# Performance work log

Measured on AMD Instinct MI355X. Metric: run time of the kernel, lower is better.

Reference implementation:

```python
import jax, jax.numpy as jnp
import numpy as np

NEG = -10000.0
EPS = 1e-5

B, N, H, DEPTH = 4096, 64, 128, 3
H2 = H // 2


def setup_inputs() -> dict:
    key = jax.random.key(0)
    k1, k2, k3 = jax.random.split(key, 3)
    hidden_states = jax.random.normal(k1, (B, N, H), dtype=jnp.float32)
    li_vector_num = jax.random.randint(k2, (B,), 0, N + 1, dtype=jnp.int32)
    Ws = jax.random.normal(k3, (DEPTH, H, H2), dtype=jnp.float32) * (1.0 / np.sqrt(H))
    bs = jnp.zeros((DEPTH, H2), dtype=jnp.float32)
    ln_w = jnp.ones((DEPTH, H2), dtype=jnp.float32)
    ln_b = jnp.zeros((DEPTH, H2), dtype=jnp.float32)
    return {"hidden_states": hidden_states, "li_vector_num": li_vector_num,
            "Ws": Ws, "bs": bs, "ln_w": ln_w, "ln_b": ln_b}


def _subgraph(hidden_states, Ws, bs, ln_w, ln_b, li_vector_num):
    b, n, h = hidden_states.shape
    # padding mask: -10000 for invalid vectors (i >= li_vector_num), per polyline
    pad = jnp.where(jnp.arange(n)[None, :] >= li_vector_num[:, None], NEG, 0.0)
    pad = pad.astype(hidden_states.dtype)[:, :, None]  # [B,N,1]
    hs = hidden_states
    for l in range(Ws.shape[0]):
        # MLP: linear -> layernorm -> relu
        x = jnp.einsum('bnh,hk->bnk', hs, Ws[l]) + bs[l]
        mu = jnp.mean(x, axis=-1, keepdims=True)
        var = jnp.mean((x - mu) ** 2, axis=-1, keepdims=True)
        x = ln_w[l] * (x - mu) * jax.lax.rsqrt(var + EPS) + ln_b[l]
        enc = jax.nn.relu(x)  # [B,N,H2]
        m = enc + pad  # masked encoded states
        # leave-one-out max over vector dim via top-2 trick (replaces O(N^2) loop)
        top2 = jax.lax.top_k(jnp.swapaxes(m, 1, 2), 2)[0]  # [B,H2,2]
        top1b = top2[..., 0][:, None, :]  # [B,1,H2]
        top2b = top2[..., 1][:, None, :]  # [B,1,H2]
        loo = jnp.where(m == top1b, top2b, top1b)  # max over i != j
        loo = jnp.maximum(loo, m + NEG)            # faithful: j itself at -10000
        loo = jnp.maximum(loo, 0.0)                # torch.max(max_hidden, zeros)
        hs = jnp.concatenate([enc, loo], axis=-1)  # [B,N,H]
    return jnp.max(hs, axis=1)  # [B,H]


def reference(hidden_states, li_vector_num, Ws, bs, ln_w, ln_b):
    return _subgraph(hidden_states, Ws, bs, ln_w, ln_b, li_vector_num)
```

## Files before the change

kernel.cpp:

```cpp
#include <hip/hip_runtime.h>
#include <hip/hip_bf16.h>

#define NEGV (-10000.0f)
#define EPSV (1e-5f)
#define NINF (-3.4e38f)

typedef __attribute__((ext_vector_type(8))) short short8;
typedef __attribute__((ext_vector_type(4))) float floatx4;

constexpr int Bsz = 4096, Nv = 64, Hd = 128, DEPTH = 3, H2 = 64;
constexpr int ESTR = 72;

struct alignas(8) BH4 { __hip_bfloat162 a, b; };

__device__ __forceinline__ unsigned short f2b(float f) {
    unsigned int u = __builtin_bit_cast(unsigned int, f);
    u += 0x7fffu + ((u >> 16) & 1u);
    return (unsigned short)(u >> 16);
}
__device__ __forceinline__ float b2f(short s) {
    unsigned int u = ((unsigned int)(unsigned short)s) << 16;
    return __builtin_bit_cast(float, u);
}

template <int CTRL>
__device__ __forceinline__ float dpp_add(float v) {
    int y = __builtin_amdgcn_update_dpp(0, __builtin_bit_cast(int, v), CTRL, 0xf, 0xf, true);
    return v + __builtin_bit_cast(float, y);
}
__device__ __forceinline__ float sum16(float v) {
    v = dpp_add<0xB1>(v);
    v = dpp_add<0x4E>(v);
    v = dpp_add<0x124>(v);
    v = dpp_add<0x128>(v);
    return v;
}

__device__ __forceinline__ void t2ins(float& t1, float& t2, float v) {
    float lo = fminf(t1, v); t1 = fmaxf(t1, v); t2 = fmaxf(t2, lo);
}
__device__ __forceinline__ void t2merge(float& t1, float& t2, float o1, float o2) {
    float lo = fminf(t1, o1); t1 = fmaxf(t1, o1); t2 = fmaxf(fmaxf(t2, o2), lo);
}

__global__ void prep_w(const float* __restrict__ Ws, unsigned short* __restrict__ wt) {
    int idx = blockIdx.x * 256 + threadIdx.x;
    if (idx < DEPTH * 8192) {
        int l = idx >> 13, o = idx & 8191;
        int j = o & 7, q = (o >> 3) & 63, hi = (o >> 9) & 3, kt = o >> 11;
        int k = kt * 32 + hi * 8 + j;
        int srccol = (q & 15) * 4 + (q >> 4);
        wt[idx] = f2b(Ws[l * 8192 + k * 64 + srccol]);
    }
}

__global__ __launch_bounds__(256, 3)
void subgraph_kernel(const float* __restrict__ hidden, const int* __restrict__ lvn,
                     const unsigned short* __restrict__ wt,
                     const float* __restrict__ bsv, const float* __restrict__ lnw,
                     const float* __restrict__ lnb, float* __restrict__ out)
{
    __shared__ __hip_bfloat16 encs[2][4][16][ESTR];
    __shared__ float fbuf3[4][4][2][2][64];
    __shared__ float2 mbuf[2][64];
    __shared__ float obuf[2][4][128];

    const int t = threadIdx.x;
    const int lane = t & 63, wid = t >> 6;
    const int b0 = blockIdx.x * 2;
    const int lr = lane & 15, hi = lane >> 4;
    const int L0 = lvn[b0], L1 = lvn[b0 + 1];
    const int arow = wid * 16 + lr;
    const float mA[2] = {(arow >= L0) ? NEGV : 0.0f, (arow >= L1) ? NEGV : 0.0f};

    const float4* ab0 = (const float4*)(hidden + (size_t)b0 * Nv * Hd);
    const float4* ab1 = ab0 + (Nv * Hd) / 4;

    float em[2][4], lm[2][4];

#pragma unroll
    for (int l = 0; l < DEPTH; ++l) {
        const short8* wfrag = (const short8*)(wt + l * 8192);

        short8 af[2][4];
        if (l == 0) {
#pragma unroll
            for (int p = 0; p < 2; ++p) {
                const float4* ab = p ? ab1 : ab0;
#pragma unroll
                for (int kt = 0; kt < 4; ++kt) {
                    int fi = arow * 32 + kt * 8 + hi * 2;
                    float4 f0 = ab[fi], f1 = ab[fi + 1];
                    union { short8 s; __hip_bfloat162 h[4]; } u;
                    u.h[0] = __float22bfloat162_rn(make_float2(f0.x, f0.y));
                    u.h[1] = __float22bfloat162_rn(make_float2(f0.z, f0.w));
                    u.h[2] = __float22bfloat162_rn(make_float2(f1.x, f1.y));
                    u.h[3] = __float22bfloat162_rn(make_float2(f1.z, f1.w));
                    af[p][kt] = u.s;
                }
            }
        } else {
#pragma unroll
            for (int p = 0; p < 2; ++p) {
                af[p][0] = *(const short8*)&encs[p][wid][lr][hi * 8];
                af[p][1] = *(const short8*)&encs[p][wid][lr][32 + hi * 8];
            }
#pragma unroll
            for (int kt = 2; kt < 4; ++kt) {
                int base = (kt - 2) * 16 + hi * 4;
#pragma unroll
                for (int p = 0; p < 2; ++p) {
                    const float4* mq = (const float4*)mbuf[p];
                    float4 q0 = mq[base + 0], q1 = mq[base + 1];
                    float4 q2 = mq[base + 2], q3 = mq[base + 3];
                    float f1s[8] = {q0.x, q0.z, q1.x, q1.z, q2.x, q2.z, q3.x, q3.z};
                    float f2s[8] = {q0.y, q0.w, q1.y, q1.w, q2.y, q2.w, q3.y, q3.w};
                    short8 e = *(const short8*)&encs[p][wid][lr][(kt - 2) * 32 + hi * 8];
                    float lo[8];
#pragma unroll
                    for (int j = 0; j < 8; ++j) {
                        float m = b2f(e[j]) + mA[p];
                        float sel = (m == f1s[j]) ? f2s[j] : f1s[j];
                        lo[j] = fmaxf(sel, 0.0f);
                    }
                    union { short8 s; __hip_bfloat162 h[4]; } u;
                    u.h[0] = __float22bfloat162_rn(make_float2(lo[0], lo[1]));
                    u.h[1] = __float22bfloat162_rn(make_float2(lo[2], lo[3]));
                    u.h[2] = __float22bfloat162_rn(make_float2(lo[4], lo[5]));
                    u.h[3] = __float22bfloat162_rn(make_float2(lo[6], lo[7]));
                    af[p][kt] = u.s;
                }
            }
        }

        floatx4 acc[2][4];
#pragma unroll
        for (int p = 0; p < 2; ++p)
#pragma unroll
            for (int ct = 0; ct < 4; ++ct) { floatx4 z = {0.f, 0.f, 0.f, 0.f}; acc[p][ct] = z; }
#pragma unroll
        for (int kt = 0; kt < 4; ++kt)
#pragma unroll
            for (int ct = 0; ct < 4; ++ct) {
                short8 bf = wfrag[(kt * 4 + hi) * 64 + ct * 16 + lr];
                acc[0][ct] = __builtin_amdgcn_mfma_f32_16x16x32_bf16(af[0][kt], bf, acc[0][ct], 0, 0, 0);
                acc[1][ct] = __builtin_amdgcn_mfma_f32_16x16x32_bf16(af[1][kt], bf, acc[1][ct], 0, 0, 0);
            }

        float4 bias = *(const float4*)(bsv + l * H2 + 4 * lr);
        float4 gwv  = *(const float4*)(lnw + l * H2 + 4 * lr);
        float4 gbv  = *(const float4*)(lnb + l * H2 + 4 * lr);
#pragma unroll
        for (int p = 0; p < 2; ++p)
#pragma unroll
            for (int reg = 0; reg < 4; ++reg) {
                float x0 = acc[p][0][reg] + bias.x;
                float x1 = acc[p][1][reg] + bias.y;
                float x2 = acc[p][2][reg] + bias.z;
                float x3 = acc[p][3][reg] + bias.w;
                float s = sum16((x0 + x1) + (x2 + x3));
                float q = sum16((x0 * x0 + x1 * x1) + (x2 * x2 + x3 * x3));
                float mu  = s * (1.0f / 64.0f);
                float var = fmaxf(q * (1.0f / 64.0f) - mu * mu, 0.0f);
                float rstd = rsqrtf(var + EPSV);
                acc[p][0][reg] = fmaxf(gwv.x * (x0 - mu) * rstd + gbv.x, 0.0f);
                acc[p][1][reg] = fmaxf(gwv.y * (x1 - mu) * rstd + gbv.y, 0.0f);
                acc[p][2][reg] = fmaxf(gwv.z * (x2 - mu) * rstd + gbv.z, 0.0f);
                acc[p][3][reg] = fmaxf(gwv.w * (x3 - mu) * rstd + gbv.w, 0.0f);
            }

        if (l < DEPTH - 1) {
#pragma unroll
            for (int p = 0; p < 2; ++p) {
                const int Lp = p ? L1 : L0;
                float t1v[4] = {NINF, NINF, NINF, NINF}, t2v[4] = {NINF, NINF, NINF, NINF};
#pragma unroll
                for (int reg = 0; reg < 4; ++reg) {
                    float mk = ((wid * 16 + hi * 4 + reg) >= Lp) ? NEGV : 0.0f;
                    BH4 we;
                    we.a = __float22bfloat162_rn(make_float2(acc[p][0][reg], acc[p][1][reg]));
                    we.b = __float22bfloat162_rn(make_float2(acc[p][2][reg], acc[p][3][reg]));
                    *(BH4*)&encs[p][wid][hi * 4 + reg][4 * lr] = we;
                    t2ins(t1v[0], t2v[0], __bfloat162float(we.a.x) + mk);
                    t2ins(t1v[1], t2v[1], __bfloat162float(we.a.y) + mk);
                    t2ins(t1v[2], t2v[2], __bfloat162float(we.b.x) + mk);
                    t2ins(t1v[3], t2v[3], __bfloat162float(we.b.y) + mk);
                }
                *(float4*)&fbuf3[wid][hi][p][0][4 * lr] = make_float4(t1v[0], t1v[1], t1v[2], t1v[3]);
                *(float4*)&fbuf3[wid][hi][p][1][4 * lr] = make_float4(t2v[0], t2v[1], t2v[2], t2v[3]);
            }
        } else {
#pragma unroll
            for (int p = 0; p < 2; ++p) {
                const int Lp = p ? L1 : L0;
                float t1v[4], t2v[4];
#pragma unroll
                for (int ct = 0; ct < 4; ++ct) {
                    float a1 = NINF, a2 = NINF;
#pragma unroll
                    for (int reg = 0; reg < 4; ++reg) {
                        float mk = ((wid * 16 + hi * 4 + reg) >= Lp) ? NEGV : 0.0f;
                        t2ins(a1, a2, acc[p][ct][reg] + mk);
                    }
                    t1v[ct] = a1; t2v[ct] = a2;
                }
                *(float4*)&fbuf3[wid][hi][p][0][4 * lr] = make_float4(t1v[0], t1v[1], t1v[2], t1v[3]);
                *(float4*)&fbuf3[wid][hi][p][1][4 * lr] = make_float4(t2v[0], t2v[1], t2v[2], t2v[3]);
            }
        }
        __syncthreads();

        if (t < 128) {
            int p = t >> 6, c = t & 63;
            float m1 = NINF, m2 = NINF;
#pragma unroll
            for (int w = 0; w < 4; ++w)
#pragma unroll
                for (int h = 0; h < 4; ++h)
                    t2merge(m1, m2, fbuf3[w][h][p][0][c], fbuf3[w][h][p][1][c]);
            mbuf[p][c] = make_float2(m1, m2);
        }
        __syncthreads();

        if (l == DEPTH - 1) {
#pragma unroll
            for (int p = 0; p < 2; ++p) {
                const int Lp = p ? L1 : L0;
                const float4* mq = (const float4*)mbuf[p];
                float4 h0 = mq[2 * lr], h1 = mq[2 * lr + 1];
                float f1v[4] = {h0.x, h0.z, h1.x, h1.z};
                float f2v[4] = {h0.y, h0.w, h1.y, h1.w};
#pragma unroll
                for (int ct = 0; ct < 4; ++ct) {
                    float e0 = NINF, l0 = NINF;
#pragma unroll
                    for (int reg = 0; reg < 4; ++reg) {
                        float e = acc[p][ct][reg];
                        e0 = fmaxf(e0, e);
                        float mk = ((wid * 16 + hi * 4 + reg) >= Lp) ? NEGV : 0.0f;
                        float mv = e + mk;
                        float v = (mv == f1v[ct]) ? f2v[ct] : f1v[ct];
                        l0 = fmaxf(l0, fmaxf(v, 0.0f));
                    }
                    e0 = fmaxf(e0, __shfl_xor(e0, 16, 64));
                    e0 = fmaxf(e0, __shfl_xor(e0, 32, 64));
                    l0 = fmaxf(l0, __shfl_xor(l0, 16, 64));
                    l0 = fmaxf(l0, __shfl_xor(l0, 32, 64));
                    em[p][ct] = e0; lm[p][ct] = l0;
                }
            }
        }
    }

    if (hi == 0) {
#pragma unroll
        for (int p = 0; p < 2; ++p) {
            *(float4*)&obuf[p][wid][4 * lr]      = make_float4(em[p][0], em[p][1], em[p][2], em[p][3]);
            *(float4*)&obuf[p][wid][64 + 4 * lr] = make_float4(lm[p][0], lm[p][1], lm[p][2], lm[p][3]);
        }
    }
    __syncthreads();
    {
        int p = t >> 7, h = t & 127;
        float v = fmaxf(fmaxf(obuf[p][0][h], obuf[p][1][h]), fmaxf(obuf[p][2][h], obuf[p][3][h]));
        out[(size_t)(b0 + p) * Hd + h] = v;
    }
}

extern "C" void kernel_launch(void* const* d_in, const int* in_sizes, int n_in,
                              void* d_out, int out_size, void* d_ws, size_t ws_size,
                              hipStream_t stream) {
    const float* hidden = (const float*)d_in[0];
    const int*   lvn    = (const int*)d_in[1];
    const float* Ws     = (const float*)d_in[2];
    const float* bs     = (const float*)d_in[3];
    const float* lnwp   = (const float*)d_in[4];
    const float* lnbp   = (const float*)d_in[5];
    unsigned short* wt  = (unsigned short*)d_ws;
    float* outp = (float*)d_out;

    prep_w<<<(DEPTH * 8192 + 255) / 256, 256, 0, stream>>>(Ws, wt);
    subgraph_kernel<<<Bsz / 2, 256, 0, stream>>>(hidden, lvn, wt, bs, lnwp, lnbp, outp);
}
```

Measured before the change: 63.73 us.

## Track argmax row for leave-one-out max and simplify final-layer reduction

The top-2 reduction now also records the row index holding the maximum, and the merged per-column maxima are stored pre-rounded to bf16 with the ReLU already applied. Building the leave-one-out operand then only needs an index compare and a byte permute, replacing per-element bf16 decode, mask add, float compare and re-rounding. In the last layer the leave-one-out max collapses to a plain masked max, because the max over rows of the leave-one-out values is just the overall top-1 (or 0 after the ReLU). That removes the second top-2 pass, the shuffles and the extra output staging buffer and barrier. Tie handling shifts from value equality to index identity, and the top-2 is now taken on fp32 values rather than bf16-rounded ones, which can change results slightly.

```diff
diff --git a/kernel.cpp b/kernel.cpp
--- a/kernel.cpp
+++ b/kernel.cpp
@@ -17,10 +17,6 @@
     unsigned int u = __builtin_bit_cast(unsigned int, f);
     u += 0x7fffu + ((u >> 16) & 1u);
     return (unsigned short)(u >> 16);
-}
-__device__ __forceinline__ float b2f(short s) {
-    unsigned int u = ((unsigned int)(unsigned short)s) << 16;
-    return __builtin_bit_cast(float, u);
 }
 
 template <int CTRL>
@@ -36,11 +32,13 @@
     return v;
 }
 
-__device__ __forceinline__ void t2ins(float& t1, float& t2, float v) {
-    float lo = fminf(t1, v); t1 = fmaxf(t1, v); t2 = fmaxf(t2, lo);
-}
-__device__ __forceinline__ void t2merge(float& t1, float& t2, float o1, float o2) {
-    float lo = fminf(t1, o1); t1 = fmaxf(t1, o1); t2 = fmaxf(fmaxf(t2, o2), lo);
+__device__ __forceinline__ void t2insIdx(float& t1, float& t2, unsigned& i1,
+                                         float v, unsigned iv) {
+    bool c = v > t1;
+    float lo = fminf(t1, v);
+    t1 = fmaxf(t1, v);
+    i1 = c ? iv : i1;
+    t2 = fmaxf(t2, lo);
 }
 
 __global__ void prep_w(const float* __restrict__ Ws, unsigned short* __restrict__ wt) {
@@ -61,23 +59,27 @@
                      const float* __restrict__ lnb, float* __restrict__ out)
 {
     __shared__ __hip_bfloat16 encs[2][4][16][ESTR];
-    __shared__ float fbuf3[4][4][2][2][64];
-    __shared__ float2 mbuf[2][64];
-    __shared__ float obuf[2][4][128];
+    __shared__ float fbuf3[4][4][2][3][64];
+    __shared__ float apk[2][64][2];
+    __shared__ unsigned short aidx[2][64];
 
     const int t = threadIdx.x;
     const int lane = t & 63, wid = t >> 6;
     const int b0 = blockIdx.x * 2;
     const int lr = lane & 15, hi = lane >> 4;
     const int L0 = lvn[b0], L1 = lvn[b0 + 1];
-    const int arow = wid * 16 + lr;
-    const float mA[2] = {(arow >= L0) ? NEGV : 0.0f, (arow >= L1) ? NEGV : 0.0f};
+    const unsigned myrow = wid * 16 + lr;
+
+    float madd[2][4];
+#pragma unroll
+    for (int p = 0; p < 2; ++p)
+#pragma unroll
+        for (int reg = 0; reg < 4; ++reg)
+            madd[p][reg] = ((int)(wid * 16 + hi * 4 + reg) >= (p ? L1 : L0)) ? NEGV : 0.0f;
 
     const float4* ab0 = (const float4*)(hidden + (size_t)b0 * Nv * Hd);
     const float4* ab1 = ab0 + (Nv * Hd) / 4;
 
-    float em[2][4], lm[2][4];
-
 #pragma unroll
     for (int l = 0; l < DEPTH; ++l) {
         const short8* wfrag = (const short8*)(wt + l * 8192);
@@ -89,7 +91,7 @@
                 const float4* ab = p ? ab1 : ab0;
 #pragma unroll
                 for (int kt = 0; kt < 4; ++kt) {
-                    int fi = arow * 32 + kt * 8 + hi * 2;
+                    int fi = (int)myrow * 32 + kt * 8 + hi * 2;
                     float4 f0 = ab[fi], f1 = ab[fi + 1];
                     union { short8 s; __hip_bfloat162 h[4]; } u;
                     u.h[0] = __float22bfloat162_rn(make_float2(f0.x, f0.y));
@@ -107,28 +109,33 @@
             }
 #pragma unroll
             for (int kt = 2; kt < 4; ++kt) {
-                int base = (kt - 2) * 16 + hi * 4;
+                int cbase = (kt - 2) * 32 + hi * 8;
 #pragma unroll
                 for (int p = 0; p < 2; ++p) {
-                    const float4* mq = (const float4*)mbuf[p];
-                    float4 q0 = mq[base + 0], q1 = mq[base + 1];
-                    float4 q2 = mq[base + 2], q3 = mq[base + 3];
-                    float f1s[8] = {q0.x, q0.z, q1.x, q1.z, q2.x, q2.z, q3.x, q3.z};
-                    float f2s[8] = {q0.y, q0.w, q1.y, q1.w, q2.y, q2.w, q3.y, q3.w};
-                    short8 e = *(const short8*)&encs[p][wid][lr][(kt - 2) * 32 + hi * 8];
-                    float lo[8];
-#pragma unroll
-                    for (int j = 0; j < 8; ++j) {
-                        float m = b2f(e[j]) + mA[p];
-                        float sel = (m == f1s[j]) ? f2s[j] : f1s[j];
-                        lo[j] = fmaxf(sel, 0.0f);
+                    short8 ar = *(const short8*)&aidx[p][cbase];
+                    const float4* ap = (const float4*)&apk[p][0][0];
+                    int fb = cbase >> 1;
+                    float4 q0 = ap[fb], q1 = ap[fb + 1], q2 = ap[fb + 2], q3 = ap[fb + 3];
+                    unsigned pk1s[8] = {
+                        __builtin_bit_cast(unsigned, q0.x), __builtin_bit_cast(unsigned, q0.z),
+                        __builtin_bit_cast(unsigned, q1.x), __builtin_bit_cast(unsigned, q1.z),
+                        __builtin_bit_cast(unsigned, q2.x), __builtin_bit_cast(unsigned, q2.z),
+                        __builtin_bit_cast(unsigned, q3.x), __builtin_bit_cast(unsigned, q3.z)};
+                    unsigned pk2s[8] = {
+                        __builtin_bit_cast(unsigned, q0.y), __builtin_bit_cast(unsigned, q0.w),
+                        __builtin_bit_cast(unsigned, q1.y), __builtin_bit_cast(unsigned, q1.w),
+                        __builtin_bit_cast(unsigned, q2.y), __builtin_bit_cast(unsigned, q2.w),
+                        __builtin_bit_cast(unsigned, q3.y), __builtin_bit_cast(unsigned, q3.w)};
+                    union { short8 s; unsigned u[4]; } uu;
+#pragma unroll
+                    for (int j2 = 0; j2 < 4; ++j2) {
+                        unsigned s0 = ((unsigned)(unsigned short)ar[2 * j2]     == myrow)
+                                      ? pk2s[2 * j2]     : pk1s[2 * j2];
+                        unsigned s1 = ((unsigned)(unsigned short)ar[2 * j2 + 1] == myrow)
+                                      ? pk2s[2 * j2 + 1] : pk1s[2 * j2 + 1];
+                        uu.u[j2] = __builtin_amdgcn_perm(s1, s0, 0x05040100u);
                     }
-                    union { short8 s; __hip_bfloat162 h[4]; } u;
-                    u.h[0] = __float22bfloat162_rn(make_float2(lo[0], lo[1]));
-                    u.h[1] = __float22bfloat162_rn(make_float2(lo[2], lo[3]));
-                    u.h[2] = __float22bfloat162_rn(make_float2(lo[4], lo[5]));
-                    u.h[3] = __float22bfloat162_rn(make_float2(lo[6], lo[7]));
-                    af[p][kt] = u.s;
+                    af[p][kt] = uu.s;
                 }
             }
         }
@@ -172,98 +179,81 @@
         if (l < DEPTH - 1) {
 #pragma unroll
             for (int p = 0; p < 2; ++p) {
-                const int Lp = p ? L1 : L0;
                 float t1v[4] = {NINF, NINF, NINF, NINF}, t2v[4] = {NINF, NINF, NINF, NINF};
+                unsigned i1v[4] = {0, 0, 0, 0};
 #pragma unroll
                 for (int reg = 0; reg < 4; ++reg) {
-                    float mk = ((wid * 16 + hi * 4 + reg) >= Lp) ? NEGV : 0.0f;
                     BH4 we;
                     we.a = __float22bfloat162_rn(make_float2(acc[p][0][reg], acc[p][1][reg]));
                     we.b = __float22bfloat162_rn(make_float2(acc[p][2][reg], acc[p][3][reg]));
                     *(BH4*)&encs[p][wid][hi * 4 + reg][4 * lr] = we;
-                    t2ins(t1v[0], t2v[0], __bfloat162float(we.a.x) + mk);
-                    t2ins(t1v[1], t2v[1], __bfloat162float(we.a.y) + mk);
-                    t2ins(t1v[2], t2v[2], __bfloat162float(we.b.x) + mk);
-                    t2ins(t1v[3], t2v[3], __bfloat162float(we.b.y) + mk);
+                    float mk = madd[p][reg];
+                    unsigned rowi = wid * 16 + hi * 4 + reg;
+                    t2insIdx(t1v[0], t2v[0], i1v[0], acc[p][0][reg] + mk, rowi);
+                    t2insIdx(t1v[1], t2v[1], i1v[1], acc[p][1][reg] + mk, rowi);
+                    t2insIdx(t1v[2], t2v[2], i1v[2], acc[p][2][reg] + mk, rowi);
+                    t2insIdx(t1v[3], t2v[3], i1v[3], acc[p][3][reg] + mk, rowi);
                 }
                 *(float4*)&fbuf3[wid][hi][p][0][4 * lr] = make_float4(t1v[0], t1v[1], t1v[2], t1v[3]);
                 *(float4*)&fbuf3[wid][hi][p][1][4 * lr] = make_float4(t2v[0], t2v[1], t2v[2], t2v[3]);
-            }
+                *(float4*)&fbuf3[wid][hi][p][2][4 * lr] = make_float4(
+                    __builtin_bit_cast(float, i1v[0]), __builtin_bit_cast(float, i1v[1]),
+                    __builtin_bit_cast(float, i1v[2]), __builtin_bit_cast(float, i1v[3]));
+            }
+            __syncthreads();
+
+            if (t < 128) {
+                int p = t >> 6, c = t & 63;
+                float m1 = NINF, m2 = NINF; unsigned a1 = 0;
+#pragma unroll
+                for (int w = 0; w < 4; ++w)
+#pragma unroll
+                    for (int h = 0; h < 4; ++h) {
+                        float o1 = fbuf3[w][h][p][0][c], o2 = fbuf3[w][h][p][1][c];
+                        unsigned io = __builtin_bit_cast(unsigned, fbuf3[w][h][p][2][c]);
+                        bool cg = o1 > m1;
+                        float lo = fminf(m1, o1);
+                        m1 = fmaxf(m1, o1);
+                        a1 = cg ? io : a1;
+                        m2 = fmaxf(fmaxf(m2, o2), lo);
+                    }
+                float F1 = fmaxf(m1, 0.0f), F2 = fmaxf(m2, 0.0f);
+                apk[p][c][0] = __builtin_bit_cast(float, (unsigned)f2b(F1));
+                apk[p][c][1] = __builtin_bit_cast(float, (unsigned)f2b(F2));
+                aidx[p][c] = (unsigned short)a1;
+            }
+            __syncthreads();
         } else {
 #pragma unroll
             for (int p = 0; p < 2; ++p) {
-                const int Lp = p ? L1 : L0;
-                float t1v[4], t2v[4];
+                float t1v[4], em4[4];
 #pragma unroll
                 for (int ct = 0; ct < 4; ++ct) {
-                    float a1 = NINF, a2 = NINF;
-#pragma unroll
-                    for (int reg = 0; reg < 4; ++reg) {
-                        float mk = ((wid * 16 + hi * 4 + reg) >= Lp) ? NEGV : 0.0f;
-                        t2ins(a1, a2, acc[p][ct][reg] + mk);
+                    float a = acc[p][ct][0], b = acc[p][ct][1];
+                    float c2 = acc[p][ct][2], d = acc[p][ct][3];
+                    em4[ct] = fmaxf(fmaxf(a, b), fmaxf(c2, d));
+                    t1v[ct] = fmaxf(fmaxf(a + madd[p][0], b + madd[p][1]),
+                                    fmaxf(c2 + madd[p][2], d + madd[p][3]));
+                }
+                *(float4*)&fbuf3[wid][hi][p][0][4 * lr] = make_float4(t1v[0], t1v[1], t1v[2], t1v[3]);
+                *(float4*)&fbuf3[wid][hi][p][1][4 * lr] = make_float4(em4[0], em4[1], em4[2], em4[3]);
+            }
+            __syncthreads();
+
+            if (t < 128) {
+                int p = t >> 6, c = t & 63;
+                float mm = NINF, me = NINF;
+#pragma unroll
+                for (int w = 0; w < 4; ++w)
+#pragma unroll
+                    for (int h = 0; h < 4; ++h) {
+                        mm = fmaxf(mm, fbuf3[w][h][p][0][c]);
+                        me = fmaxf(me, fbuf3[w][h][p][1][c]);
                     }
-                    t1v[ct] = a1; t2v[ct] = a2;
-                }
-                *(float4*)&fbuf3[wid][hi][p][0][4 * lr] = make_float4(t1v[0], t1v[1], t1v[2], t1v[3]);
-                *(float4*)&fbuf3[wid][hi][p][1][4 * lr] = make_float4(t2v[0], t2v[1], t2v[2], t2v[3]);
+                out[(size_t)(b0 + p) * Hd + c]      = me;
+                out[(size_t)(b0 + p) * Hd + 64 + c] = fmaxf(mm, 0.0f);
             }
         }
-        __syncthreads();
-
-        if (t < 128) {
-            int p = t >> 6, c = t & 63;
-            float m1 = NINF, m2 = NINF;
-#pragma unroll
-            for (int w = 0; w < 4; ++w)
-#pragma unroll
-                for (int h = 0; h < 4; ++h)
-                    t2merge(m1, m2, fbuf3[w][h][p][0][c], fbuf3[w][h][p][1][c]);
-            mbuf[p][c] = make_float2(m1, m2);
-        }
-        __syncthreads();
-
-        if (l == DEPTH - 1) {
-#pragma unroll
-            for (int p = 0; p < 2; ++p) {
-                const int Lp = p ? L1 : L0;
-                const float4* mq = (const float4*)mbuf[p];
-                float4 h0 = mq[2 * lr], h1 = mq[2 * lr + 1];
-                float f1v[4] = {h0.x, h0.z, h1.x, h1.z};
-                float f2v[4] = {h0.y, h0.w, h1.y, h1.w};
-#pragma unroll
-                for (int ct = 0; ct < 4; ++ct) {
-                    float e0 = NINF, l0 = NINF;
-#pragma unroll
-                    for (int reg = 0; reg < 4; ++reg) {
-                        float e = acc[p][ct][reg];
-                        e0 = fmaxf(e0, e);
-                        float mk = ((wid * 16 + hi * 4 + reg) >= Lp) ? NEGV : 0.0f;
-                        float mv = e + mk;
-                        float v = (mv == f1v[ct]) ? f2v[ct] : f1v[ct];
-                        l0 = fmaxf(l0, fmaxf(v, 0.0f));
-                    }
-                    e0 = fmaxf(e0, __shfl_xor(e0, 16, 64));
-                    e0 = fmaxf(e0, __shfl_xor(e0, 32, 64));
-                    l0 = fmaxf(l0, __shfl_xor(l0, 16, 64));
-                    l0 = fmaxf(l0, __shfl_xor(l0, 32, 64));
-                    em[p][ct] = e0; lm[p][ct] = l0;
-                }
-            }
-        }
-    }
-
-    if (hi == 0) {
-#pragma unroll
-        for (int p = 0; p < 2; ++p) {
-            *(float4*)&obuf[p][wid][4 * lr]      = make_float4(em[p][0], em[p][1], em[p][2], em[p][3]);
-            *(float4*)&obuf[p][wid][64 + 4 * lr] = make_float4(lm[p][0], lm[p][1], lm[p][2], lm[p][3]);
-        }
-    }
-    __syncthreads();
-    {
-        int p = t >> 7, h = t & 127;
-        float v = fmaxf(fmaxf(obuf[p][0][h], obuf[p][1][h]), fmaxf(obuf[p][2][h], obuf[p][3][h]));
-        out[(size_t)(b0 + p) * Hd + h] = v;
     }
 }
 
```

Result: faster. 56.21 us, median of 2 (-11.8%).
